# Kernel optimization log

Hardware: AMD Instinct MI355X
Metric: run time of the kernel (lower is better)

The kernel has to match this reference:

```python
import jax, jax.numpy as jnp
import numpy as np


def setup_inputs() -> dict:
    key = jax.random.key(0)
    ks = jax.random.split(key, 7)
    t, e, h = 2048, 512, 8
    s = 0.02
    return {
        "x": jax.random.normal(ks[0], (t, e), jnp.float32),
        "y": jax.random.normal(ks[1], (t, e), jnp.float32),
        "Wk": jax.random.normal(ks[2], (e, e * h), jnp.float32) * s,
        "Wq": jax.random.normal(ks[3], (e, e * h), jnp.float32) * s,
        "Wv": jax.random.normal(ks[4], (e, e * h), jnp.float32) * s,
        "Wu": jax.random.normal(ks[5], (e * h, e), jnp.float32) * s,
        "bu": jnp.zeros((e,), jnp.float32),
    }


def reference(x, y, Wk, Wq, Wv, Wu, bu):
    t, e = x.shape
    h = Wk.shape[1] // e
    scale = e ** (-0.25)
    # projections -> [h, t, e] (head dim equals emb in this 'wide' attention)
    k = (x @ Wk).reshape(t, h, e).transpose(1, 0, 2) * scale
    q = (y @ Wq).reshape(t, h, e).transpose(1, 0, 2) * scale
    v = (x @ Wv).reshape(t, h, e).transpose(1, 0, 2)
    # scores [h, t, t]
    dot = jnp.einsum('hte,hse->hts', q, k)
    attn = jax.nn.softmax(dot, axis=-1)
    out = jnp.einsum('hts,hse->hte', attn, v)          # [h, t, e]
    out = out.transpose(1, 0, 2).reshape(t, h * e)     # [t, h*e]
    return (out @ Wu + bu)[None]                       # [1, t, e] (b=1 in original)
```

## Files before the change

### kernel.cpp

```cpp
#include <hip/hip_runtime.h>
#include <hip/hip_bf16.h>
#include <stdint.h>

#define T_SEQ 2048
#define EMB   512
#define NH    8
#define HEAD_ALL 4096

typedef __attribute__((ext_vector_type(8))) short short8;
typedef __attribute__((ext_vector_type(4))) float f32x4;

__device__ __forceinline__ unsigned short f2b(float f) {
    __hip_bfloat16 h = __float2bfloat16(f);
    return *reinterpret_cast<unsigned short*>(&h);
}
__device__ __forceinline__ float b2f(unsigned short u) {
    return __uint_as_float(((unsigned)u) << 16);
}
__device__ __forceinline__ void gload_lds16(const void* g, void* l) {
    __builtin_amdgcn_global_load_lds((__attribute__((address_space(1))) void*)(void*)(g),
                                     (__attribute__((address_space(3))) void*)(l), 16, 0, 0);
}
__device__ __forceinline__ void wg_barrier() {
    asm volatile("" ::: "memory");
    __builtin_amdgcn_s_barrier();
    asm volatile("" ::: "memory");
}

__global__ void cvt_bf16_kernel(const float* __restrict__ in, unsigned short* __restrict__ out, int n8) {
    int i = blockIdx.x * 256 + threadIdx.x;
    if (i >= n8) return;
    const f32x4* p = (const f32x4*)in + 2*(size_t)i;
    f32x4 a = p[0], b = p[1];
    uint4 o;
    o.x = (unsigned)f2b(a[0]) | ((unsigned)f2b(a[1]) << 16);
    o.y = (unsigned)f2b(a[2]) | ((unsigned)f2b(a[3]) << 16);
    o.z = (unsigned)f2b(b[0]) | ((unsigned)f2b(b[1]) << 16);
    o.w = (unsigned)f2b(b[2]) | ((unsigned)f2b(b[3]) << 16);
    *((uint4*)out + i) = o;
}

__global__ void transpose_cvt3_f32(const float* __restrict__ w0, const float* __restrict__ w1,
                                   const float* __restrict__ w2, unsigned short* __restrict__ out,
                                   int R, int C, long outS) {
    __shared__ unsigned short t[64][66];
    const int z = blockIdx.z;
    const float* in = (z == 0) ? w0 : ((z == 1) ? w1 : w2);
    unsigned short* ob = out + (long)z * outS;
    const int tid = threadIdx.x;
    const int r0 = blockIdx.y * 64, c0 = blockIdx.x * 64;
#pragma unroll
    for (int it = 0; it < 4; ++it) {
        int flat = it * 256 + tid;
        int r = flat >> 4, c4 = flat & 15;
        f32x4 v = *(const f32x4*)(in + (long)(r0 + r) * C + c0 + c4 * 4);
#pragma unroll
        for (int w = 0; w < 4; ++w) t[r][c4 * 4 + w] = f2b(v[w]);
    }
    __syncthreads();
#pragma unroll
    for (int it = 0; it < 2; ++it) {
        int flat = it * 256 + tid;
        int rr = flat >> 3, c8 = flat & 7;
        unsigned u[4];
#pragma unroll
        for (int w = 0; w < 4; ++w) {
            unsigned short a = t[c8 * 8 + 2 * w][rr];
            unsigned short b = t[c8 * 8 + 2 * w + 1][rr];
            u[w] = (unsigned)a | ((unsigned)b << 16);
        }
        *(uint4*)(ob + (long)(c0 + rr) * R + r0 + c8 * 8) = make_uint4(u[0], u[1], u[2], u[3]);
    }
}

__global__ void transpose_bf16(const unsigned short* __restrict__ in, unsigned short* __restrict__ out,
                               int R, int C, long inS, long outS) {
    __shared__ unsigned short t[64][66];
    const unsigned short* ib = in + (long)blockIdx.z * inS;
    unsigned short* ob = out + (long)blockIdx.z * outS;
    const int tid = threadIdx.x;
    const int r0 = blockIdx.y * 64, c0 = blockIdx.x * 64;
#pragma unroll
    for (int it = 0; it < 2; ++it) {
        int flat = it * 256 + tid;
        int r = flat >> 3, c8 = flat & 7;
        uint4 v = *(const uint4*)(ib + (long)(r0 + r) * C + c0 + c8 * 8);
        unsigned u[4] = {v.x, v.y, v.z, v.w};
#pragma unroll
        for (int w = 0; w < 4; ++w) {
            t[r][c8 * 8 + 2 * w]     = (unsigned short)(u[w] & 0xffff);
            t[r][c8 * 8 + 2 * w + 1] = (unsigned short)(u[w] >> 16);
        }
    }
    __syncthreads();
#pragma unroll
    for (int it = 0; it < 2; ++it) {
        int flat = it * 256 + tid;
        int rr = flat >> 3, c8 = flat & 7;
        unsigned u[4];
#pragma unroll
        for (int w = 0; w < 4; ++w)
            u[w] = (unsigned)t[c8 * 8 + 2 * w][rr] | ((unsigned)t[c8 * 8 + 2 * w + 1][rr] << 16);
        *(uint4*)(ob + (long)(c0 + rr) * R + r0 + c8 * 8) = make_uint4(u[0], u[1], u[2], u[3]);
    }
}

template<int R_>
__device__ __forceinline__ void stage2(const unsigned short* __restrict__ src, int kfull,
                                       short* ldsbase, int i, int tid, int wid) {
#pragma unroll
    for (int s = 0; s < 2; ++s) {
        const int ii = i + s;
        const int r = ii * 64 + (tid >> 3);
        const int d = (tid & 7) * 16;
        const int sc = (d ^ ((r & 7) << 4)) >> 1;
        gload_lds16(src + (long)r * kfull + sc, ldsbase + ii * 4096 + wid * 512);
    }
}

template<int BM, int BN, int KTILES, int MODE>
__global__ __launch_bounds__(512, 2)
void gemm8p(const unsigned short* __restrict__ A, const unsigned short* __restrict__ A2,
            const unsigned short* __restrict__ B, void* __restrict__ Cout,
            float* __restrict__ rpart,
            int kfull, float alpha, long As, long Bs, long Cs, int ldc)
{
    static_assert(KTILES >= 3, "pipeline needs >=3 K-tiles");
    constexpr int ATILE = BM * 64;
    constexpr int BTILE = BN * 64;
    constexpr int LA = BM / 64;
    constexpr int LB = BN / 64;
    constexpr int MF = BM / 32;
    constexpr int NF = BN / 64;
    constexpr int MFP = MF / 4;
    constexpr int LDSN = 2 * (ATILE + BTILE);

    __shared__ __align__(16) short lds[LDSN + ((MODE == 4) ? 2 * BM : 0)];

    const int tid = threadIdx.x;
    const int wid = tid >> 6, lane = tid & 63;
    const int wm = wid >> 2, wn = wid & 3;
    const int fr = lane & 15, fq = lane >> 4;

    const int nwg = gridDim.x * gridDim.y * gridDim.z;
    int flat = blockIdx.x + gridDim.x * (blockIdx.y + gridDim.y * blockIdx.z);
    flat = (flat & 7) * (nwg >> 3) + (flat >> 3);
    const int bx = flat % gridDim.x;
    const int rem = flat / gridDim.x;
    const int by = rem % gridDim.y;
    const long batch = rem / gridDim.y;

    const int bm = by * BM, bn = bx * BN;

    const unsigned short* Ab;
    const unsigned short* Bb;
    int koff = 0;
    if constexpr (MODE == 1) { Ab = (batch == 2) ? A2 : A; Bb = B + batch * Bs; }
    else if constexpr (MODE == 3) { Ab = A; Bb = B; koff = (int)batch * (KTILES * 64); }
    else { Ab = A + batch * As; Bb = B + batch * Bs; }

    const unsigned short* Ag = Ab + (long)bm * kfull + koff;
    const unsigned short* Bg = Bb + (long)bn * kfull + koff;

    f32x4 acc[MF][NF];
#pragma unroll
    for (int i = 0; i < MF; i++)
#pragma unroll
        for (int j = 0; j < NF; j++) acc[i][j] = 0.f;

    float* rinv = (float*)(lds + LDSN);
    if constexpr (MODE == 4) {
        for (int r = tid; r < BM; r += 512) {
            float s = 0.f;
#pragma unroll
            for (int i = 0; i < 32; ++i) s += rpart[((long)batch * 32 + i) * T_SEQ + bm + r];
            rinv[r] = 1.0f / s;
        }
        asm volatile("s_waitcnt lgkmcnt(0)" ::: "memory");
    }

#pragma unroll
    for (int i = 0; i < LA; i += 2) stage2<BM>(Ag, kfull, lds, i, tid, wid);
#pragma unroll
    for (int i = 0; i < LB; i += 2) stage2<BN>(Bg, kfull, lds + 2 * ATILE, i, tid, wid);
#pragma unroll
    for (int i = 0; i < LB; i += 2) stage2<BN>(Bg + 64, kfull, lds + 2 * ATILE + BTILE, i, tid, wid);
    if constexpr (LB == 4) asm volatile("s_waitcnt vmcnt(4)" ::: "memory");
    else                   asm volatile("s_waitcnt vmcnt(2)" ::: "memory");
    wg_barrier();

#pragma unroll 2
    for (int t = 0; t < KTILES; ++t) {
        short* la  = lds + (t & 1) * ATILE;
        short* laN = lds + ((t + 1) & 1) * ATILE;
        short* lb  = lds + 2 * ATILE + (t & 1) * BTILE;
        const int kA = (t + 1) * 64;
        const int kB = (t + 2) * 64;

        short8 bfrag[NF][2];
#pragma unroll
        for (int q = 0; q < 4; ++q) {
            if (q == 0) {
#pragma unroll
                for (int nf = 0; nf < NF; ++nf)
#pragma unroll
                    for (int kk = 0; kk < 2; ++kk) {
                        const int r = wn * (BN / 4) + nf * 16 + fr;
                        const int cb = kk * 64 + fq * 16;
                        bfrag[nf][kk] = *(const short8*)(lb + r * 64 + ((cb ^ ((r & 7) << 4)) >> 1));
                    }
            }
            short8 afrag[MFP][2];
#pragma unroll
            for (int mf = 0; mf < MFP; ++mf)
#pragma unroll
                for (int kk = 0; kk < 2; ++kk) {
                    const int r = wm * (BM / 2) + q * (BM / 8) + mf * 16 + fr;
                    const int cb = kk * 64 + fq * 16;
                    afrag[mf][kk] = *(const short8*)(la + r * 64 + ((cb ^ ((r & 7) << 4)) >> 1));
                }
            if (t + 1 < KTILES) {
                if (q == 0) stage2<BM>(Ag + kA, kfull, laN, 0, tid, wid);
                if (q == 1 && LA == 4) stage2<BM>(Ag + kA, kfull, laN, 2, tid, wid);
            }
            if (t + 2 < KTILES) {
                if (q == 2) stage2<BN>(Bg + kB, kfull, lb, 0, tid, wid);
                if (q == 3 && LB == 4) stage2<BN>(Bg + kB, kfull, lb, 2, tid, wid);
            }
            wg_barrier();
            __builtin_amdgcn_s_setprio(1);
#pragma unroll
            for (int mf = 0; mf < MFP; ++mf)
#pragma unroll
                for (int nf = 0; nf < NF; ++nf)
#pragma unroll
                    for (int kk = 0; kk < 2; ++kk)
                        acc[q * MFP + mf][nf] = __builtin_amdgcn_mfma_f32_16x16x32_bf16(
                            afrag[mf][kk], bfrag[nf][kk], acc[q * MFP + mf][nf], 0, 0, 0);
            __builtin_amdgcn_s_setprio(0);
            if (q == 3) {
                if (t + 2 < KTILES) {
                    if constexpr (LB == 4) asm volatile("s_waitcnt vmcnt(4)" ::: "memory");
                    else                   asm volatile("s_waitcnt vmcnt(2)" ::: "memory");
                } else {
                    asm volatile("s_waitcnt vmcnt(0)" ::: "memory");
                }
            }
            wg_barrier();
        }
    }

#pragma unroll
    for (int m = 0; m < MF; ++m)
#pragma unroll
        for (int j = 0; j < 4; ++j) {
            const int row = bm + wm * (BM / 2) + m * 16 + fq * 4 + j;
            float rowsum = 0.f;
#pragma unroll
            for (int n = 0; n < NF; ++n) {
                const int col = bn + wn * (BN / 4) + n * 16 + fr;
                const float v = acc[m][n][j] * alpha;
                if constexpr (MODE == 1) {
                    unsigned short* C = (unsigned short*)Cout + batch * Cs;
                    C[(long)(col >> 9) * ((long)T_SEQ * EMB) + (long)row * EMB + (col & 511)] = f2b(v);
                } else if constexpr (MODE == 2) {
                    unsigned short* C = (unsigned short*)Cout + batch * Cs;
                    const unsigned short us = f2b(__expf(v));
                    C[(long)row * ldc + col] = us;
                    rowsum += b2f(us);
                } else if constexpr (MODE == 3) {
                    float* C = (float*)Cout + batch * ((long)T_SEQ * EMB);
                    C[(long)row * ldc + col] = v;
                } else {
                    unsigned short* C = (unsigned short*)Cout + batch * Cs;
                    C[(long)row * ldc + col] = f2b(v * rinv[row - bm]);
                }
            }
            if constexpr (MODE == 2) {
                rowsum += __shfl_xor(rowsum, 1);
                rowsum += __shfl_xor(rowsum, 2);
                rowsum += __shfl_xor(rowsum, 4);
                rowsum += __shfl_xor(rowsum, 8);
                if (fr == 0)
                    rpart[(((long)batch * 8 + bx) * 4 + wn) * T_SEQ + row] = rowsum;
            }
        }
}

__global__ void reduce_bias(const float* __restrict__ part, const float* __restrict__ bias,
                            float* __restrict__ out) {
    const int i = blockIdx.x * 256 + threadIdx.x;
    const long stride4 = (long)T_SEQ * EMB / 4;
    const f32x4* p = (const f32x4*)part;
    f32x4 s = p[i];
#pragma unroll
    for (int sl = 1; sl < 8; ++sl) s += p[i + sl * stride4];
    f32x4 b = *(const f32x4*)(bias + ((i * 4) % EMB));
    *((f32x4*)out + i) = s + b;
}

extern "C" void kernel_launch(void* const* d_in, const int* in_sizes, int n_in,
                              void* d_out, int out_size, void* d_ws, size_t ws_size,
                              hipStream_t stream)
{
    const float* x  = (const float*)d_in[0];
    const float* y  = (const float*)d_in[1];
    const float* Wk = (const float*)d_in[2];
    const float* Wq = (const float*)d_in[3];
    const float* Wv = (const float*)d_in[4];
    const float* Wu = (const float*)d_in[5];
    const float* bu = (const float*)d_in[6];
    char* ws = (char*)d_ws;
    const size_t MB = 1024ull * 1024ull;

    unsigned short* Sb   = (unsigned short*)(ws + 0);
    unsigned short* xb   = (unsigned short*)(ws + 0);
    unsigned short* yb   = (unsigned short*)(ws + 2 * MB);
    unsigned short* WT3  = (unsigned short*)(ws + 4 * MB);
    unsigned short* PRJ  = (unsigned short*)(ws + 48 * MB);
    unsigned short* Vb   = (unsigned short*)(ws + 48 * MB);
    unsigned short* Kb   = (unsigned short*)(ws + 64 * MB);
    unsigned short* Qb   = (unsigned short*)(ws + 80 * MB);
    unsigned short* WuT  = (unsigned short*)(ws + 96 * MB);
    unsigned short* VTb  = (unsigned short*)(ws + 100 * MB);
    unsigned short* Ob   = (unsigned short*)(ws + 116 * MB);
    float*          rpart= (float*)(ws + 132 * MB);
    float*          part = (float*)(ws + 0);

    const float scale2 = 0.04419417382415922f;
    const long TE = (long)T_SEQ * EMB;

    cvt_bf16_kernel<<<dim3(512), dim3(256), 0, stream>>>(x, xb, T_SEQ * EMB / 8);
    cvt_bf16_kernel<<<dim3(512), dim3(256), 0, stream>>>(y, yb, T_SEQ * EMB / 8);
    transpose_cvt3_f32<<<dim3(HEAD_ALL / 64, EMB / 64, 3), dim3(256), 0, stream>>>(
        Wv, Wk, Wq, WT3, EMB, HEAD_ALL, (long)2 * MB);
    transpose_cvt3_f32<<<dim3(EMB / 64, HEAD_ALL / 64, 1), dim3(256), 0, stream>>>(
        Wu, nullptr, nullptr, WuT, HEAD_ALL, EMB, 0);

    gemm8p<256, 256, 8, 1><<<dim3(HEAD_ALL / 256, T_SEQ / 256, 3), 512, 0, stream>>>(
        xb, yb, WT3, PRJ, nullptr, EMB, 1.f, 0, (long)2 * MB, (long)8 * MB, 0);

    transpose_bf16<<<dim3(EMB / 64, T_SEQ / 64, NH), dim3(256), 0, stream>>>(
        Vb, VTb, T_SEQ, EMB, TE, TE);

    gemm8p<256, 256, 8, 2><<<dim3(T_SEQ / 256, T_SEQ / 256, NH), 512, 0, stream>>>(
        Qb, nullptr, Kb, Sb, rpart, EMB, scale2, TE, TE, (long)T_SEQ * T_SEQ, T_SEQ);

    gemm8p<128, 256, 32, 4><<<dim3(EMB / 256, T_SEQ / 128, NH), 512, 0, stream>>>(
        Sb, nullptr, VTb, Ob, rpart, T_SEQ, 1.f, (long)T_SEQ * T_SEQ, TE, (long)EMB, HEAD_ALL);

    gemm8p<256, 128, 8, 3><<<dim3(EMB / 128, T_SEQ / 256, 8), 512, 0, stream>>>(
        Ob, nullptr, WuT, part, nullptr, HEAD_ALL, 1.f, 0, 0, 0, EMB);

    reduce_bias<<<dim3(T_SEQ * EMB / 4 / 256), dim3(256), 0, stream>>>(part, bu, (float*)d_out);
}
```

Before: 178.3 us.

## Switch to 32x32 MFMA, fuse V transpose and row-sum, retile output GEMM

The GEMM core moves from 16x16x32 to 32x32x16 bf16 MFMA fragments with a new register layout. The V projection is written transposed straight from the projection GEMM, so the separate transpose kernel goes away. Softmax row sums are now computed inside the PV GEMM from the bf16 P fragments it already loads, which removes the rpart partial buffer and its reduction. The two input conversions are merged into one launch, and the output projection uses 128x128 tiles with a 4-way K split and higher occupancy. In exchange, the transposed V stores are strided and the extra row-sum adds sit in the inner loop.

```diff
diff --git a/kernel.cpp b/kernel.cpp
--- a/kernel.cpp
+++ b/kernel.cpp
@@ -7,15 +7,13 @@
 #define NH    8
 #define HEAD_ALL 4096
 
-typedef __attribute__((ext_vector_type(8))) short short8;
-typedef __attribute__((ext_vector_type(4))) float f32x4;
+typedef __attribute__((ext_vector_type(8)))  short short8;
+typedef __attribute__((ext_vector_type(4)))  float f32x4;
+typedef __attribute__((ext_vector_type(16))) float f32x16;
 
 __device__ __forceinline__ unsigned short f2b(float f) {
     __hip_bfloat16 h = __float2bfloat16(f);
     return *reinterpret_cast<unsigned short*>(&h);
-}
-__device__ __forceinline__ float b2f(unsigned short u) {
-    return __uint_as_float(((unsigned)u) << 16);
 }
 __device__ __forceinline__ void gload_lds16(const void* g, void* l) {
     __builtin_amdgcn_global_load_lds((__attribute__((address_space(1))) void*)(void*)(g),
@@ -26,17 +24,28 @@
     __builtin_amdgcn_s_barrier();
     asm volatile("" ::: "memory");
 }
-
-__global__ void cvt_bf16_kernel(const float* __restrict__ in, unsigned short* __restrict__ out, int n8) {
+__device__ __forceinline__ float sum8bf16(short8 v) {
+    uint4 u; __builtin_memcpy(&u, &v, 16);
+    float s = __uint_as_float(u.x << 16) + __uint_as_float(u.x & 0xffff0000u);
+    s += __uint_as_float(u.y << 16) + __uint_as_float(u.y & 0xffff0000u);
+    s += __uint_as_float(u.z << 16) + __uint_as_float(u.z & 0xffff0000u);
+    s += __uint_as_float(u.w << 16) + __uint_as_float(u.w & 0xffff0000u);
+    return s;
+}
+
+__global__ void cvt_bf16_2(const float* __restrict__ a, const float* __restrict__ b,
+                           unsigned short* __restrict__ oa, unsigned short* __restrict__ ob, int n8) {
+    const float* in = blockIdx.y ? b : a;
+    unsigned short* out = blockIdx.y ? ob : oa;
     int i = blockIdx.x * 256 + threadIdx.x;
     if (i >= n8) return;
-    const f32x4* p = (const f32x4*)in + 2*(size_t)i;
-    f32x4 a = p[0], b = p[1];
+    const f32x4* p = (const f32x4*)in + 2 * (size_t)i;
+    f32x4 va = p[0], vb = p[1];
     uint4 o;
-    o.x = (unsigned)f2b(a[0]) | ((unsigned)f2b(a[1]) << 16);
-    o.y = (unsigned)f2b(a[2]) | ((unsigned)f2b(a[3]) << 16);
-    o.z = (unsigned)f2b(b[0]) | ((unsigned)f2b(b[1]) << 16);
-    o.w = (unsigned)f2b(b[2]) | ((unsigned)f2b(b[3]) << 16);
+    o.x = (unsigned)f2b(va[0]) | ((unsigned)f2b(va[1]) << 16);
+    o.y = (unsigned)f2b(va[2]) | ((unsigned)f2b(va[3]) << 16);
+    o.z = (unsigned)f2b(vb[0]) | ((unsigned)f2b(vb[1]) << 16);
+    o.w = (unsigned)f2b(vb[2]) | ((unsigned)f2b(vb[3]) << 16);
     *((uint4*)out + i) = o;
 }
 
@@ -73,38 +82,6 @@
     }
 }
 
-__global__ void transpose_bf16(const unsigned short* __restrict__ in, unsigned short* __restrict__ out,
-                               int R, int C, long inS, long outS) {
-    __shared__ unsigned short t[64][66];
-    const unsigned short* ib = in + (long)blockIdx.z * inS;
-    unsigned short* ob = out + (long)blockIdx.z * outS;
-    const int tid = threadIdx.x;
-    const int r0 = blockIdx.y * 64, c0 = blockIdx.x * 64;
-#pragma unroll
-    for (int it = 0; it < 2; ++it) {
-        int flat = it * 256 + tid;
-        int r = flat >> 3, c8 = flat & 7;
-        uint4 v = *(const uint4*)(ib + (long)(r0 + r) * C + c0 + c8 * 8);
-        unsigned u[4] = {v.x, v.y, v.z, v.w};
-#pragma unroll
-        for (int w = 0; w < 4; ++w) {
-            t[r][c8 * 8 + 2 * w]     = (unsigned short)(u[w] & 0xffff);
-            t[r][c8 * 8 + 2 * w + 1] = (unsigned short)(u[w] >> 16);
-        }
-    }
-    __syncthreads();
-#pragma unroll
-    for (int it = 0; it < 2; ++it) {
-        int flat = it * 256 + tid;
-        int rr = flat >> 3, c8 = flat & 7;
-        unsigned u[4];
-#pragma unroll
-        for (int w = 0; w < 4; ++w)
-            u[w] = (unsigned)t[c8 * 8 + 2 * w][rr] | ((unsigned)t[c8 * 8 + 2 * w + 1][rr] << 16);
-        *(uint4*)(ob + (long)(c0 + rr) * R + r0 + c8 * 8) = make_uint4(u[0], u[1], u[2], u[3]);
-    }
-}
-
 template<int R_>
 __device__ __forceinline__ void stage2(const unsigned short* __restrict__ src, int kfull,
                                        short* ldsbase, int i, int tid, int wid) {
@@ -118,11 +95,10 @@
     }
 }
 
-template<int BM, int BN, int KTILES, int MODE>
-__global__ __launch_bounds__(512, 2)
+template<int BM, int BN, int KTILES, int MODE, int MINW = 2>
+__global__ __launch_bounds__(512, MINW)
 void gemm8p(const unsigned short* __restrict__ A, const unsigned short* __restrict__ A2,
             const unsigned short* __restrict__ B, void* __restrict__ Cout,
-            float* __restrict__ rpart,
             int kfull, float alpha, long As, long Bs, long Cs, int ldc)
 {
     static_assert(KTILES >= 3, "pipeline needs >=3 K-tiles");
@@ -130,17 +106,16 @@
     constexpr int BTILE = BN * 64;
     constexpr int LA = BM / 64;
     constexpr int LB = BN / 64;
-    constexpr int MF = BM / 32;
-    constexpr int NF = BN / 64;
-    constexpr int MFP = MF / 4;
-    constexpr int LDSN = 2 * (ATILE + BTILE);
-
-    __shared__ __align__(16) short lds[LDSN + ((MODE == 4) ? 2 * BM : 0)];
+    constexpr int MB32 = (BM / 2) / 32;
+    constexpr int NB32 = (BN / 4) / 32;
+
+    __shared__ __align__(16) short lds[2 * (ATILE + BTILE)];
+    __shared__ float rbuf[8][(MODE == 4) ? MB32 : 1][32];
 
     const int tid = threadIdx.x;
     const int wid = tid >> 6, lane = tid & 63;
     const int wm = wid >> 2, wn = wid & 3;
-    const int fr = lane & 15, fq = lane >> 4;
+    const int l31 = lane & 31, hi = lane >> 5;
 
     const int nwg = gridDim.x * gridDim.y * gridDim.z;
     int flat = blockIdx.x + gridDim.x * (blockIdx.y + gridDim.y * blockIdx.z);
@@ -155,29 +130,22 @@
     const unsigned short* Ab;
     const unsigned short* Bb;
     int koff = 0;
-    if constexpr (MODE == 1) { Ab = (batch == 2) ? A2 : A; Bb = B + batch * Bs; }
+    if constexpr (MODE == 1) { Ab = (batch == 1) ? A2 : A; Bb = B + batch * Bs; }
     else if constexpr (MODE == 3) { Ab = A; Bb = B; koff = (int)batch * (KTILES * 64); }
     else { Ab = A + batch * As; Bb = B + batch * Bs; }
 
     const unsigned short* Ag = Ab + (long)bm * kfull + koff;
     const unsigned short* Bg = Bb + (long)bn * kfull + koff;
 
-    f32x4 acc[MF][NF];
-#pragma unroll
-    for (int i = 0; i < MF; i++)
-#pragma unroll
-        for (int j = 0; j < NF; j++) acc[i][j] = 0.f;
-
-    float* rinv = (float*)(lds + LDSN);
-    if constexpr (MODE == 4) {
-        for (int r = tid; r < BM; r += 512) {
-            float s = 0.f;
-#pragma unroll
-            for (int i = 0; i < 32; ++i) s += rpart[((long)batch * 32 + i) * T_SEQ + bm + r];
-            rinv[r] = 1.0f / s;
-        }
-        asm volatile("s_waitcnt lgkmcnt(0)" ::: "memory");
-    }
+    f32x16 acc[MB32][NB32];
+#pragma unroll
+    for (int i = 0; i < MB32; i++)
+#pragma unroll
+        for (int j = 0; j < NB32; j++) acc[i][j] = 0.f;
+
+    float rowacc[MB32];
+#pragma unroll
+    for (int i = 0; i < MB32; i++) rowacc[i] = 0.f;
 
 #pragma unroll
     for (int i = 0; i < LA; i += 2) stage2<BM>(Ag, kfull, lds, i, tid, wid);
@@ -197,28 +165,29 @@
         const int kA = (t + 1) * 64;
         const int kB = (t + 2) * 64;
 
-        short8 bfrag[NF][2];
+        short8 bfrag[NB32][4];
 #pragma unroll
         for (int q = 0; q < 4; ++q) {
             if (q == 0) {
 #pragma unroll
-                for (int nf = 0; nf < NF; ++nf)
-#pragma unroll
-                    for (int kk = 0; kk < 2; ++kk) {
-                        const int r = wn * (BN / 4) + nf * 16 + fr;
-                        const int cb = kk * 64 + fq * 16;
-                        bfrag[nf][kk] = *(const short8*)(lb + r * 64 + ((cb ^ ((r & 7) << 4)) >> 1));
+                for (int nb = 0; nb < NB32; ++nb)
+#pragma unroll
+                    for (int ks = 0; ks < 4; ++ks) {
+                        const int r = wn * (BN / 4) + nb * 32 + l31;
+                        const int cb = ks * 32 + hi * 16;
+                        bfrag[nb][ks] = *(const short8*)(lb + r * 64 + ((cb ^ ((r & 7) << 4)) >> 1));
                     }
             }
-            short8 afrag[MFP][2];
-#pragma unroll
-            for (int mf = 0; mf < MFP; ++mf)
-#pragma unroll
-                for (int kk = 0; kk < 2; ++kk) {
-                    const int r = wm * (BM / 2) + q * (BM / 8) + mf * 16 + fr;
-                    const int cb = kk * 64 + fq * 16;
-                    afrag[mf][kk] = *(const short8*)(la + r * 64 + ((cb ^ ((r & 7) << 4)) >> 1));
-                }
+            short8 afrag[MB32];
+#pragma unroll
+            for (int p = 0; p < MB32; ++p) {
+                const int idx = q * MB32 + p;
+                const int mblk = idx >> 2, ks = idx & 3;
+                const int r = wm * (BM / 2) + mblk * 32 + l31;
+                const int cb = ks * 32 + hi * 16;
+                afrag[p] = *(const short8*)(la + r * 64 + ((cb ^ ((r & 7) << 4)) >> 1));
+                if constexpr (MODE == 4) rowacc[mblk] += sum8bf16(afrag[p]);
+            }
             if (t + 1 < KTILES) {
                 if (q == 0) stage2<BM>(Ag + kA, kfull, laN, 0, tid, wid);
                 if (q == 1 && LA == 4) stage2<BM>(Ag + kA, kfull, laN, 2, tid, wid);
@@ -230,13 +199,14 @@
             wg_barrier();
             __builtin_amdgcn_s_setprio(1);
 #pragma unroll
-            for (int mf = 0; mf < MFP; ++mf)
-#pragma unroll
-                for (int nf = 0; nf < NF; ++nf)
-#pragma unroll
-                    for (int kk = 0; kk < 2; ++kk)
-                        acc[q * MFP + mf][nf] = __builtin_amdgcn_mfma_f32_16x16x32_bf16(
-                            afrag[mf][kk], bfrag[nf][kk], acc[q * MFP + mf][nf], 0, 0, 0);
+            for (int p = 0; p < MB32; ++p) {
+                const int idx = q * MB32 + p;
+                const int mblk = idx >> 2, ks = idx & 3;
+#pragma unroll
+                for (int nb = 0; nb < NB32; ++nb)
+                    acc[mblk][nb] = __builtin_amdgcn_mfma_f32_32x32x16_bf16(
+                        afrag[p], bfrag[nb][ks], acc[mblk][nb], 0, 0, 0);
+            }
             __builtin_amdgcn_s_setprio(0);
             if (q == 3) {
                 if (t + 2 < KTILES) {
@@ -250,39 +220,40 @@
         }
     }
 
-#pragma unroll
-    for (int m = 0; m < MF; ++m)
-#pragma unroll
-        for (int j = 0; j < 4; ++j) {
-            const int row = bm + wm * (BM / 2) + m * 16 + fq * 4 + j;
-            float rowsum = 0.f;
-#pragma unroll
-            for (int n = 0; n < NF; ++n) {
-                const int col = bn + wn * (BN / 4) + n * 16 + fr;
-                const float v = acc[m][n][j] * alpha;
+    if constexpr (MODE == 4) {
+#pragma unroll
+        for (int mb = 0; mb < MB32; ++mb) {
+            float rs = rowacc[mb] + __shfl_xor(rowacc[mb], 32);
+            if (lane < 32) rbuf[wid][mb][l31] = 1.0f / rs;
+        }
+    }
+
+#pragma unroll
+    for (int mb = 0; mb < MB32; ++mb)
+#pragma unroll
+        for (int reg = 0; reg < 16; ++reg) {
+            const int rloc = (reg & 3) + 8 * (reg >> 2) + 4 * hi;
+            const int row = bm + wm * (BM / 2) + mb * 32 + rloc;
+#pragma unroll
+            for (int nb = 0; nb < NB32; ++nb) {
+                const int col = bn + wn * (BN / 4) + nb * 32 + l31;
+                const float v = acc[mb][nb][reg] * alpha;
                 if constexpr (MODE == 1) {
                     unsigned short* C = (unsigned short*)Cout + batch * Cs;
-                    C[(long)(col >> 9) * ((long)T_SEQ * EMB) + (long)row * EMB + (col & 511)] = f2b(v);
+                    if (batch == 2)
+                        C[(long)(col >> 9) * ((long)T_SEQ * EMB) + (long)(col & 511) * T_SEQ + row] = f2b(v);
+                    else
+                        C[(long)(col >> 9) * ((long)T_SEQ * EMB) + (long)row * EMB + (col & 511)] = f2b(v);
                 } else if constexpr (MODE == 2) {
                     unsigned short* C = (unsigned short*)Cout + batch * Cs;
-                    const unsigned short us = f2b(__expf(v));
-                    C[(long)row * ldc + col] = us;
-                    rowsum += b2f(us);
+                    C[(long)row * ldc + col] = f2b(__expf(v));
                 } else if constexpr (MODE == 3) {
                     float* C = (float*)Cout + batch * ((long)T_SEQ * EMB);
                     C[(long)row * ldc + col] = v;
                 } else {
                     unsigned short* C = (unsigned short*)Cout + batch * Cs;
-                    C[(long)row * ldc + col] = f2b(v * rinv[row - bm]);
+                    C[(long)row * ldc + col] = f2b(v * rbuf[wid][mb][rloc]);
                 }
-            }
-            if constexpr (MODE == 2) {
-                rowsum += __shfl_xor(rowsum, 1);
-                rowsum += __shfl_xor(rowsum, 2);
-                rowsum += __shfl_xor(rowsum, 4);
-                rowsum += __shfl_xor(rowsum, 8);
-                if (fr == 0)
-                    rpart[(((long)batch * 8 + bx) * 4 + wn) * T_SEQ + row] = rowsum;
             }
         }
 }
@@ -294,7 +265,7 @@
     const f32x4* p = (const f32x4*)part;
     f32x4 s = p[i];
 #pragma unroll
-    for (int sl = 1; sl < 8; ++sl) s += p[i + sl * stride4];
+    for (int sl = 1; sl < 4; ++sl) s += p[i + sl * stride4];
     f32x4 b = *(const f32x4*)(bias + ((i * 4) % EMB));
     *((f32x4*)out + i) = s + b;
 }
@@ -317,40 +288,33 @@
     unsigned short* xb   = (unsigned short*)(ws + 0);
     unsigned short* yb   = (unsigned short*)(ws + 2 * MB);
     unsigned short* WT3  = (unsigned short*)(ws + 4 * MB);
-    unsigned short* PRJ  = (unsigned short*)(ws + 48 * MB);
-    unsigned short* Vb   = (unsigned short*)(ws + 48 * MB);
     unsigned short* Kb   = (unsigned short*)(ws + 64 * MB);
     unsigned short* Qb   = (unsigned short*)(ws + 80 * MB);
-    unsigned short* WuT  = (unsigned short*)(ws + 96 * MB);
-    unsigned short* VTb  = (unsigned short*)(ws + 100 * MB);
+    unsigned short* VTb  = (unsigned short*)(ws + 96 * MB);
+    unsigned short* WuT  = (unsigned short*)(ws + 112 * MB);
     unsigned short* Ob   = (unsigned short*)(ws + 116 * MB);
-    float*          rpart= (float*)(ws + 132 * MB);
     float*          part = (float*)(ws + 0);
 
     const float scale2 = 0.04419417382415922f;
     const long TE = (long)T_SEQ * EMB;
 
-    cvt_bf16_kernel<<<dim3(512), dim3(256), 0, stream>>>(x, xb, T_SEQ * EMB / 8);
-    cvt_bf16_kernel<<<dim3(512), dim3(256), 0, stream>>>(y, yb, T_SEQ * EMB / 8);
+    cvt_bf16_2<<<dim3(512, 2), dim3(256), 0, stream>>>(x, y, xb, yb, T_SEQ * EMB / 8);
     transpose_cvt3_f32<<<dim3(HEAD_ALL / 64, EMB / 64, 3), dim3(256), 0, stream>>>(
-        Wv, Wk, Wq, WT3, EMB, HEAD_ALL, (long)2 * MB);
+        Wk, Wq, Wv, WT3, EMB, HEAD_ALL, (long)2 * MB);
     transpose_cvt3_f32<<<dim3(EMB / 64, HEAD_ALL / 64, 1), dim3(256), 0, stream>>>(
         Wu, nullptr, nullptr, WuT, HEAD_ALL, EMB, 0);
 
     gemm8p<256, 256, 8, 1><<<dim3(HEAD_ALL / 256, T_SEQ / 256, 3), 512, 0, stream>>>(
-        xb, yb, WT3, PRJ, nullptr, EMB, 1.f, 0, (long)2 * MB, (long)8 * MB, 0);
-
-    transpose_bf16<<<dim3(EMB / 64, T_SEQ / 64, NH), dim3(256), 0, stream>>>(
-        Vb, VTb, T_SEQ, EMB, TE, TE);
+        xb, yb, WT3, Kb, EMB, 1.f, 0, (long)2 * MB, (long)8 * MB, 0);
 
     gemm8p<256, 256, 8, 2><<<dim3(T_SEQ / 256, T_SEQ / 256, NH), 512, 0, stream>>>(
-        Qb, nullptr, Kb, Sb, rpart, EMB, scale2, TE, TE, (long)T_SEQ * T_SEQ, T_SEQ);
+        Qb, nullptr, Kb, Sb, EMB, scale2, TE, TE, (long)T_SEQ * T_SEQ, T_SEQ);
 
     gemm8p<128, 256, 32, 4><<<dim3(EMB / 256, T_SEQ / 128, NH), 512, 0, stream>>>(
-        Sb, nullptr, VTb, Ob, rpart, T_SEQ, 1.f, (long)T_SEQ * T_SEQ, TE, (long)EMB, HEAD_ALL);
-
-    gemm8p<256, 128, 8, 3><<<dim3(EMB / 128, T_SEQ / 256, 8), 512, 0, stream>>>(
-        Ob, nullptr, WuT, part, nullptr, HEAD_ALL, 1.f, 0, 0, 0, EMB);
+        Sb, nullptr, VTb, Ob, T_SEQ, 1.f, (long)T_SEQ * T_SEQ, TE, (long)EMB, HEAD_ALL);
+
+    gemm8p<128, 128, 16, 3, 4><<<dim3(EMB / 128, T_SEQ / 128, 4), 512, 0, stream>>>(
+        Ob, nullptr, WuT, part, HEAD_ALL, 1.f, 0, 0, 0, EMB);
 
     reduce_bias<<<dim3(T_SEQ * EMB / 4 / 256), dim3(256), 0, stream>>>(part, bu, (float*)d_out);
 }
```

After: 233.4 us. 1.31x slower.

## Fuse V transpose into projection, add streaming QK kernel, retile output GEMM

Applied to the files above, without the earlier changes.

Merges the two input conversion launches into one. The projection GEMM now writes V directly in transposed layout and folds the score scale into Q, which removes the separate transpose_bf16 pass. The QK^T exp/rowsum step moves to a new sgemm_stream kernel that loads operands straight from global memory without LDS staging. The output GEMM is retiled to 128x128 with a 4-way K split, so the bias reduction sums fewer partials. Together these cut launches and intermediate traffic, but the direct-global-load score kernel may lose the operand reuse that LDS staging gave.

```diff
diff --git a/kernel.cpp b/kernel.cpp
--- a/kernel.cpp
+++ b/kernel.cpp
@@ -27,16 +27,19 @@
     asm volatile("" ::: "memory");
 }
 
-__global__ void cvt_bf16_kernel(const float* __restrict__ in, unsigned short* __restrict__ out, int n8) {
+__global__ void cvt_bf16_2(const float* __restrict__ a, const float* __restrict__ b,
+                           unsigned short* __restrict__ oa, unsigned short* __restrict__ ob, int n8) {
+    const float* in = blockIdx.y ? b : a;
+    unsigned short* out = blockIdx.y ? ob : oa;
     int i = blockIdx.x * 256 + threadIdx.x;
     if (i >= n8) return;
-    const f32x4* p = (const f32x4*)in + 2*(size_t)i;
-    f32x4 a = p[0], b = p[1];
+    const f32x4* p = (const f32x4*)in + 2 * (size_t)i;
+    f32x4 va = p[0], vb = p[1];
     uint4 o;
-    o.x = (unsigned)f2b(a[0]) | ((unsigned)f2b(a[1]) << 16);
-    o.y = (unsigned)f2b(a[2]) | ((unsigned)f2b(a[3]) << 16);
-    o.z = (unsigned)f2b(b[0]) | ((unsigned)f2b(b[1]) << 16);
-    o.w = (unsigned)f2b(b[2]) | ((unsigned)f2b(b[3]) << 16);
+    o.x = (unsigned)f2b(va[0]) | ((unsigned)f2b(va[1]) << 16);
+    o.y = (unsigned)f2b(va[2]) | ((unsigned)f2b(va[3]) << 16);
+    o.z = (unsigned)f2b(vb[0]) | ((unsigned)f2b(vb[1]) << 16);
+    o.w = (unsigned)f2b(vb[2]) | ((unsigned)f2b(vb[3]) << 16);
     *((uint4*)out + i) = o;
 }
 
@@ -73,38 +76,6 @@
     }
 }
 
-__global__ void transpose_bf16(const unsigned short* __restrict__ in, unsigned short* __restrict__ out,
-                               int R, int C, long inS, long outS) {
-    __shared__ unsigned short t[64][66];
-    const unsigned short* ib = in + (long)blockIdx.z * inS;
-    unsigned short* ob = out + (long)blockIdx.z * outS;
-    const int tid = threadIdx.x;
-    const int r0 = blockIdx.y * 64, c0 = blockIdx.x * 64;
-#pragma unroll
-    for (int it = 0; it < 2; ++it) {
-        int flat = it * 256 + tid;
-        int r = flat >> 3, c8 = flat & 7;
-        uint4 v = *(const uint4*)(ib + (long)(r0 + r) * C + c0 + c8 * 8);
-        unsigned u[4] = {v.x, v.y, v.z, v.w};
-#pragma unroll
-        for (int w = 0; w < 4; ++w) {
-            t[r][c8 * 8 + 2 * w]     = (unsigned short)(u[w] & 0xffff);
-            t[r][c8 * 8 + 2 * w + 1] = (unsigned short)(u[w] >> 16);
-        }
-    }
-    __syncthreads();
-#pragma unroll
-    for (int it = 0; it < 2; ++it) {
-        int flat = it * 256 + tid;
-        int rr = flat >> 3, c8 = flat & 7;
-        unsigned u[4];
-#pragma unroll
-        for (int w = 0; w < 4; ++w)
-            u[w] = (unsigned)t[c8 * 8 + 2 * w][rr] | ((unsigned)t[c8 * 8 + 2 * w + 1][rr] << 16);
-        *(uint4*)(ob + (long)(c0 + rr) * R + r0 + c8 * 8) = make_uint4(u[0], u[1], u[2], u[3]);
-    }
-}
-
 template<int R_>
 __device__ __forceinline__ void stage2(const unsigned short* __restrict__ src, int kfull,
                                        short* ldsbase, int i, int tid, int wid) {
@@ -118,8 +89,8 @@
     }
 }
 
-template<int BM, int BN, int KTILES, int MODE>
-__global__ __launch_bounds__(512, 2)
+template<int BM, int BN, int KTILES, int MODE, int MINW = 2>
+__global__ __launch_bounds__(512, MINW)
 void gemm8p(const unsigned short* __restrict__ A, const unsigned short* __restrict__ A2,
             const unsigned short* __restrict__ B, void* __restrict__ Cout,
             float* __restrict__ rpart,
@@ -155,7 +126,7 @@
     const unsigned short* Ab;
     const unsigned short* Bb;
     int koff = 0;
-    if constexpr (MODE == 1) { Ab = (batch == 2) ? A2 : A; Bb = B + batch * Bs; }
+    if constexpr (MODE == 1) { Ab = (batch == 1) ? A2 : A; Bb = B + batch * Bs; }
     else if constexpr (MODE == 3) { Ab = A; Bb = B; koff = (int)batch * (KTILES * 64); }
     else { Ab = A + batch * As; Bb = B + batch * Bs; }
 
@@ -253,21 +224,18 @@
 #pragma unroll
     for (int m = 0; m < MF; ++m)
 #pragma unroll
-        for (int j = 0; j < 4; ++j) {
-            const int row = bm + wm * (BM / 2) + m * 16 + fq * 4 + j;
-            float rowsum = 0.f;
-#pragma unroll
-            for (int n = 0; n < NF; ++n) {
+        for (int n = 0; n < NF; ++n)
+#pragma unroll
+            for (int j = 0; j < 4; ++j) {
+                const int row = bm + wm * (BM / 2) + m * 16 + fq * 4 + j;
                 const int col = bn + wn * (BN / 4) + n * 16 + fr;
-                const float v = acc[m][n][j] * alpha;
+                const float v = acc[m][n][j] * ((MODE == 1) ? ((batch == 1) ? alpha : 1.0f) : alpha);
                 if constexpr (MODE == 1) {
                     unsigned short* C = (unsigned short*)Cout + batch * Cs;
-                    C[(long)(col >> 9) * ((long)T_SEQ * EMB) + (long)row * EMB + (col & 511)] = f2b(v);
-                } else if constexpr (MODE == 2) {
-                    unsigned short* C = (unsigned short*)Cout + batch * Cs;
-                    const unsigned short us = f2b(__expf(v));
-                    C[(long)row * ldc + col] = us;
-                    rowsum += b2f(us);
+                    if (batch == 2)
+                        C[(long)(col >> 9) * ((long)T_SEQ * EMB) + (long)(col & 511) * T_SEQ + row] = f2b(v);
+                    else
+                        C[(long)(col >> 9) * ((long)T_SEQ * EMB) + (long)row * EMB + (col & 511)] = f2b(v);
                 } else if constexpr (MODE == 3) {
                     float* C = (float*)Cout + batch * ((long)T_SEQ * EMB);
                     C[(long)row * ldc + col] = v;
@@ -276,14 +244,66 @@
                     C[(long)row * ldc + col] = f2b(v * rinv[row - bm]);
                 }
             }
-            if constexpr (MODE == 2) {
-                rowsum += __shfl_xor(rowsum, 1);
-                rowsum += __shfl_xor(rowsum, 2);
-                rowsum += __shfl_xor(rowsum, 4);
-                rowsum += __shfl_xor(rowsum, 8);
-                if (fr == 0)
-                    rpart[(((long)batch * 8 + bx) * 4 + wn) * T_SEQ + row] = rowsum;
-            }
+}
+
+__global__ __launch_bounds__(512, 4)
+void sgemm_stream(const unsigned short* __restrict__ Q, const unsigned short* __restrict__ K,
+                  unsigned short* __restrict__ S, float* __restrict__ rpart)
+{
+    const int tid = threadIdx.x;
+    const int wid = tid >> 6, lane = tid & 63;
+    const int wm = wid >> 2, wn = wid & 3;
+    const int fr = lane & 15, fq = lane >> 4;
+    const int bx = blockIdx.x;
+    const int by = blockIdx.y;
+    const int z  = blockIdx.z;
+    const long TE = (long)T_SEQ * EMB;
+
+    const unsigned short* Ag = Q + z * TE + ((long)by * 128 + wm * 64 + fr) * EMB + fq * 8;
+    const unsigned short* Bg = K + z * TE + ((long)bx * 256 + wn * 64 + fr) * EMB + fq * 8;
+
+    f32x4 acc[4][4];
+#pragma unroll
+    for (int m = 0; m < 4; ++m)
+#pragma unroll
+        for (int n = 0; n < 4; ++n) acc[m][n] = 0.f;
+
+#pragma unroll 2
+    for (int ks = 0; ks < 16; ++ks) {
+        short8 af[4], bf[4];
+#pragma unroll
+        for (int m = 0; m < 4; ++m)
+            af[m] = *(const short8*)(Ag + (long)m * 16 * EMB + ks * 32);
+#pragma unroll
+        for (int n = 0; n < 4; ++n)
+            bf[n] = *(const short8*)(Bg + (long)n * 16 * EMB + ks * 32);
+#pragma unroll
+        for (int m = 0; m < 4; ++m)
+#pragma unroll
+            for (int n = 0; n < 4; ++n)
+                acc[m][n] = __builtin_amdgcn_mfma_f32_16x16x32_bf16(af[m], bf[n], acc[m][n], 0, 0, 0);
+    }
+
+    unsigned short* Sp = S + (long)z * T_SEQ * T_SEQ;
+#pragma unroll
+    for (int m = 0; m < 4; ++m)
+#pragma unroll
+        for (int j = 0; j < 4; ++j) {
+            const int row = by * 128 + wm * 64 + m * 16 + fq * 4 + j;
+            float rs = 0.f;
+#pragma unroll
+            for (int n = 0; n < 4; ++n) {
+                const int col = bx * 256 + wn * 64 + n * 16 + fr;
+                const unsigned short us = f2b(__expf(acc[m][n][j]));
+                Sp[(long)row * T_SEQ + col] = us;
+                rs += b2f(us);
+            }
+            rs += __shfl_xor(rs, 1);
+            rs += __shfl_xor(rs, 2);
+            rs += __shfl_xor(rs, 4);
+            rs += __shfl_xor(rs, 8);
+            if (fr == 0)
+                rpart[(((long)z * 8 + bx) * 4 + wn) * T_SEQ + row] = rs;
         }
 }
 
@@ -294,7 +314,7 @@
     const f32x4* p = (const f32x4*)part;
     f32x4 s = p[i];
 #pragma unroll
-    for (int sl = 1; sl < 8; ++sl) s += p[i + sl * stride4];
+    for (int sl = 1; sl < 4; ++sl) s += p[i + sl * stride4];
     f32x4 b = *(const f32x4*)(bias + ((i * 4) % EMB));
     *((f32x4*)out + i) = s + b;
 }
@@ -317,12 +337,10 @@
     unsigned short* xb   = (unsigned short*)(ws + 0);
     unsigned short* yb   = (unsigned short*)(ws + 2 * MB);
     unsigned short* WT3  = (unsigned short*)(ws + 4 * MB);
-    unsigned short* PRJ  = (unsigned short*)(ws + 48 * MB);
-    unsigned short* Vb   = (unsigned short*)(ws + 48 * MB);
     unsigned short* Kb   = (unsigned short*)(ws + 64 * MB);
     unsigned short* Qb   = (unsigned short*)(ws + 80 * MB);
-    unsigned short* WuT  = (unsigned short*)(ws + 96 * MB);
-    unsigned short* VTb  = (unsigned short*)(ws + 100 * MB);
+    unsigned short* VTb  = (unsigned short*)(ws + 96 * MB);
+    unsigned short* WuT  = (unsigned short*)(ws + 112 * MB);
     unsigned short* Ob   = (unsigned short*)(ws + 116 * MB);
     float*          rpart= (float*)(ws + 132 * MB);
     float*          part = (float*)(ws + 0);
@@ -330,26 +348,21 @@
     const float scale2 = 0.04419417382415922f;
     const long TE = (long)T_SEQ * EMB;
 
-    cvt_bf16_kernel<<<dim3(512), dim3(256), 0, stream>>>(x, xb, T_SEQ * EMB / 8);
-    cvt_bf16_kernel<<<dim3(512), dim3(256), 0, stream>>>(y, yb, T_SEQ * EMB / 8);
+    cvt_bf16_2<<<dim3(512, 2), dim3(256), 0, stream>>>(x, y, xb, yb, T_SEQ * EMB / 8);
     transpose_cvt3_f32<<<dim3(HEAD_ALL / 64, EMB / 64, 3), dim3(256), 0, stream>>>(
-        Wv, Wk, Wq, WT3, EMB, HEAD_ALL, (long)2 * MB);
+        Wk, Wq, Wv, WT3, EMB, HEAD_ALL, (long)2 * MB);
     transpose_cvt3_f32<<<dim3(EMB / 64, HEAD_ALL / 64, 1), dim3(256), 0, stream>>>(
         Wu, nullptr, nullptr, WuT, HEAD_ALL, EMB, 0);
 
     gemm8p<256, 256, 8, 1><<<dim3(HEAD_ALL / 256, T_SEQ / 256, 3), 512, 0, stream>>>(
-        xb, yb, WT3, PRJ, nullptr, EMB, 1.f, 0, (long)2 * MB, (long)8 * MB, 0);
-
-    transpose_bf16<<<dim3(EMB / 64, T_SEQ / 64, NH), dim3(256), 0, stream>>>(
-        Vb, VTb, T_SEQ, EMB, TE, TE);
-
-    gemm8p<256, 256, 8, 2><<<dim3(T_SEQ / 256, T_SEQ / 256, NH), 512, 0, stream>>>(
-        Qb, nullptr, Kb, Sb, rpart, EMB, scale2, TE, TE, (long)T_SEQ * T_SEQ, T_SEQ);
+        xb, yb, WT3, Kb, nullptr, EMB, scale2, 0, (long)2 * MB, (long)8 * MB, 0);
+
+    sgemm_stream<<<dim3(T_SEQ / 256, T_SEQ / 128, NH), 512, 0, stream>>>(Qb, Kb, Sb, rpart);
 
     gemm8p<128, 256, 32, 4><<<dim3(EMB / 256, T_SEQ / 128, NH), 512, 0, stream>>>(
         Sb, nullptr, VTb, Ob, rpart, T_SEQ, 1.f, (long)T_SEQ * T_SEQ, TE, (long)EMB, HEAD_ALL);
 
-    gemm8p<256, 128, 8, 3><<<dim3(EMB / 128, T_SEQ / 256, 8), 512, 0, stream>>>(
+    gemm8p<128, 128, 16, 3, 4><<<dim3(EMB / 128, T_SEQ / 128, 4), 512, 0, stream>>>(
         Ob, nullptr, WuT, part, nullptr, HEAD_ALL, 1.f, 0, 0, 0, EMB);
 
     reduce_bias<<<dim3(T_SEQ * EMB / 4 / 256), dim3(256), 0, stream>>>(part, bu, (float*)d_out);
```

Measured after the change: 285.2 us. 1.6x slower.
